# Performance work log

Measured on AMD Instinct MI355X. Metric: run time of the kernel, lower is better.

The kernel has to match this reference:

```python
import jax, jax.numpy as jnp
import numpy as np
import math

M, T, D, H, QK, K_ACT = 16, 512, 512, 512, 256, 4


def setup_inputs() -> dict:
    key = jax.random.key(0)
    ks = jax.random.split(key, 16)

    def xavier(k, shape):
        fan = shape[-1] + shape[-2]
        return jax.random.normal(k, shape, jnp.float32) * np.float32(math.sqrt(2.0 / fan))

    def bias(k, shape, fan_in):
        b = np.float32(1.0 / math.sqrt(fan_in))
        return jax.random.uniform(k, shape, jnp.float32, -b, b)

    return {
        "inputs": jax.random.normal(ks[0], (M, T, D), jnp.float32),
        # per-mechanism InputSelection params
        "Wq": xavier(ks[1], (M, QK, H)), "bq": bias(ks[2], (M, QK), H),
        "Wk": xavier(ks[3], (M, QK, D)), "bk": bias(ks[4], (M, QK), D),
        "Wv": xavier(ks[5], (M, D, D)), "bv": bias(ks[6], (M, D), D),
        # per-mechanism LSTMCell params (gate order i, f, g, o)
        "W_ih": xavier(ks[7], (M, 4 * H, D)), "b_ih": bias(ks[8], (M, 4 * H), H),
        "W_hh": xavier(ks[9], (M, 4 * H, H)), "b_hh": bias(ks[10], (M, 4 * H), H),
        # GroupLinearLayer weights for interaction attention
        "Wq_g": xavier(ks[11], (M, H, H)),
        "Wk_g": xavier(ks[12], (M, H, H)),
        "Wv_g": xavier(ks[13], (M, H, H)),
    }


def reference(inputs, Wq, bq, Wk, bk, Wv, bv, W_ih, b_ih, W_hh, b_hh, Wq_g, Wk_g, Wv_g):
    scale = 1.0 / math.sqrt(Wk.shape[1])  # 1/sqrt(key_size)
    xs = jnp.swapaxes(inputs, 0, 1)  # (T, M, D) for scan over time
    h0 = jnp.zeros((M, H), inputs.dtype)
    c0 = jnp.zeros((M, H), inputs.dtype)

    def step(carry, x_t):
        h, c = carry  # (M,H), (M,H)
        # --- InputSelection: augmented input rows are [zeros, x_t] ---
        q = jnp.einsum('mh,mqh->mq', h, Wq) + bq            # (M,QK)
        key_x = jnp.einsum('md,mkd->mk', x_t, Wk) + bk      # key of real input row
        logit0 = jnp.sum(q * bk, -1) * scale                # key of zero row == bias
        logit1 = jnp.sum(q * key_x, -1) * scale
        att = jax.nn.softmax(jnp.stack([logit0, logit1], -1), axis=-1)  # (M,2)
        val1 = jnp.einsum('md,mvd->mv', x_t, Wv) + bv       # (M,D)
        sel = att[:, 0:1] * bv + att[:, 1:2] * val1         # value of zero row == bias
        # --- top-k routing: smallest attention to the null input ---
        _, active_idx = jax.lax.top_k(-att[:, 0], K_ACT)
        mask = jnp.zeros((M,), inputs.dtype).at[active_idx].set(1.0)
        m = mask[:, None]
        # --- LSTMCell for all mechanisms, masked afterwards ---
        gates = (jnp.einsum('md,mgd->mg', sel, W_ih) + b_ih
                 + jnp.einsum('mh,mgh->mg', h, W_hh) + b_hh)  # (M,4H)
        i, f, g, o = jnp.split(gates, 4, axis=-1)
        c_new = jax.nn.sigmoid(f) * c + jax.nn.sigmoid(i) * jnp.tanh(g)
        h_new = jax.nn.sigmoid(o) * jnp.tanh(c_new)
        temp_h = m * h_new + (1 - m) * h
        new_c = m * c_new  # inactive cells are reset to zero (as in original)
        # --- interaction attention across mechanisms ---
        q2 = jnp.einsum('mh,mho->mo', temp_h, Wq_g)
        k2 = jnp.einsum('mh,mho->mo', temp_h, Wk_g)
        v2 = jnp.einsum('mh,mho->mo', temp_h, Wv_g)
        att2 = jax.nn.softmax(q2 @ k2.T, axis=1)            # (M,M), no sqrt scaling
        inter = (m * att2) @ v2                             # zero rows for inactive
        new_h = inter + (1 - m) * h + m * temp_h
        return (new_h, new_c), (new_h.reshape(-1), active_idx)

    _, (all_h, all_idx) = jax.lax.scan(step, (h0, c0), xs)
    return all_h, all_idx  # (T, M*H), (T, K_ACT)
```

## Files before the change

kernel.cpp:

```cpp
#include <hip/hip_runtime.h>

constexpr int M_ = 16, T_ = 512, D_ = 512, H_ = 512, QK_ = 256, G4_ = 2048;
constexpr float SCALE_ = 1.0f / 16.0f;

constexpr size_t KEY_OFF = 0;
constexpr size_t VAL_OFF = 2097152;
constexpr size_t H_OFF   = 6291456;
constexpr size_t C_OFF   = H_OFF + 8192;
constexpr size_t TH_OFF  = C_OFF + 8192;
constexpr size_t K2_OFF  = TH_OFF + 8192;
constexpr size_t V2_OFF  = K2_OFF + 8192;
constexpr size_t Q2_OFF  = V2_OFF + 8192;
constexpr size_t L0_OFF  = Q2_OFF + 2048;
constexpr size_t L1_OFF  = L0_OFF + 256;
constexpr size_t BAR_OFF = L1_OFF + 256;
constexpr int    BAR_WORDS = 16 * 32 + 32;

__device__ inline void load8f(const float* p, float f[8]) {
  float4 a = reinterpret_cast<const float4*>(p)[0];
  float4 b = reinterpret_cast<const float4*>(p)[1];
  f[0] = a.x; f[1] = a.y; f[2] = a.z; f[3] = a.w;
  f[4] = b.x; f[5] = b.y; f[6] = b.z; f[7] = b.w;
}

__device__ __forceinline__ float ldf(const float* p) {
  return __hip_atomic_load(p, __ATOMIC_RELAXED, __HIP_MEMORY_SCOPE_AGENT);
}
__device__ __forceinline__ void stf(float* p, float v) {
  __hip_atomic_store(p, v, __ATOMIC_RELAXED, __HIP_MEMORY_SCOPE_AGENT);
}
__device__ __forceinline__ float2 ldf2(const float* p) {
  unsigned long long u = __hip_atomic_load(
      reinterpret_cast<const unsigned long long*>(p),
      __ATOMIC_RELAXED, __HIP_MEMORY_SCOPE_AGENT);
  return __builtin_bit_cast(float2, u);
}
__device__ __forceinline__ void ld8f_cg(const float* p, float f[8]) {
  float2 a = ldf2(p), b = ldf2(p + 2), c = ldf2(p + 4), d = ldf2(p + 6);
  f[0] = a.x; f[1] = a.y; f[2] = b.x; f[3] = b.y;
  f[4] = c.x; f[5] = c.y; f[6] = d.x; f[7] = d.y;
}

__device__ inline float waveReduce(float v) {
#pragma unroll
  for (int d = 32; d > 0; d >>= 1) v += __shfl_xor(v, d);
  return v;
}

__device__ inline float sigm(float x) { return 1.f / (1.f + expf(-x)); }

__device__ __forceinline__ void gbar(float* wsf, unsigned idx) {
  unsigned* bar = reinterpret_cast<unsigned*>(wsf + BAR_OFF);
  asm volatile("s_waitcnt vmcnt(0)" ::: "memory");
  __syncthreads();
  if (threadIdx.x == 0) {
    const int sub = blockIdx.x >> 4;
    unsigned a = __hip_atomic_fetch_add(&bar[sub * 32], 1u, __ATOMIC_RELAXED,
                                        __HIP_MEMORY_SCOPE_AGENT);
    if (a == idx * 16u - 1u)
      __hip_atomic_fetch_add(&bar[512], 1u, __ATOMIC_RELAXED,
                             __HIP_MEMORY_SCOPE_AGENT);
    while (__hip_atomic_load(&bar[512], __ATOMIC_RELAXED,
                             __HIP_MEMORY_SCOPE_AGENT) < idx * 16u)
      __builtin_amdgcn_s_sleep(1);
  }
  __syncthreads();
  __builtin_amdgcn_sched_barrier(0);
}

__global__ void __launch_bounds__(256) keyval_kernel(
    const float* __restrict__ x, const float* __restrict__ Wk,
    const float* __restrict__ Wv, const float* __restrict__ bk,
    const float* __restrict__ bv, float* __restrict__ wsf) {
  __shared__ float Xs[64][33];
  __shared__ float Ws[64][33];
  int bid = blockIdx.x, tid = threadIdx.x;
  if (bid == 0) {
    for (int i = tid; i < BAR_WORDS; i += 256)
      reinterpret_cast<unsigned*>(wsf + BAR_OFF)[i] = 0u;
  }
  int m = bid / 96, r = bid % 96;
  int tt = r / 12, ot = r % 12;
  const float* xb = x + ((size_t)m * T_ + tt * 64) * D_;
  const float* wb; const float* bias; float* dst; int ld;
  if (ot < 4) {
    wb = Wk + (size_t)m * QK_ * D_ + (size_t)(ot * 64) * D_;
    bias = bk + m * QK_ + ot * 64;
    dst = wsf + KEY_OFF + ((size_t)m * T_ + tt * 64) * QK_ + ot * 64;
    ld = QK_;
  } else {
    wb = Wv + (size_t)m * D_ * D_ + (size_t)((ot - 4) * 64) * D_;
    bias = bv + m * D_ + (ot - 4) * 64;
    dst = wsf + VAL_OFF + ((size_t)m * T_ + tt * 64) * D_ + (ot - 4) * 64;
    ld = D_;
  }
  int lr = tid >> 2, lc = (tid & 3) * 8;
  int tx = tid & 15, ty = tid >> 4;
  float acc[4][4] = {};
  for (int k0 = 0; k0 < D_; k0 += 32) {
    float tmp[8];
    load8f(xb + (size_t)lr * D_ + k0 + lc, tmp);
#pragma unroll
    for (int i = 0; i < 8; ++i) Xs[lr][lc + i] = tmp[i];
    load8f(wb + (size_t)lr * D_ + k0 + lc, tmp);
#pragma unroll
    for (int i = 0; i < 8; ++i) Ws[lr][lc + i] = tmp[i];
    __syncthreads();
#pragma unroll
    for (int kk = 0; kk < 32; ++kk) {
      float xa[4], wv4[4];
#pragma unroll
      for (int a = 0; a < 4; ++a) xa[a] = Xs[ty * 4 + a][kk];
#pragma unroll
      for (int b = 0; b < 4; ++b) wv4[b] = Ws[tx * 4 + b][kk];
#pragma unroll
      for (int a = 0; a < 4; ++a)
#pragma unroll
        for (int b = 0; b < 4; ++b) acc[a][b] += xa[a] * wv4[b];
    }
    __syncthreads();
  }
#pragma unroll
  for (int b = 0; b < 4; ++b) {
    float bias_v = bias[tx * 4 + b];
#pragma unroll
    for (int a = 0; a < 4; ++a)
      dst[(size_t)(ty * 4 + a) * ld + tx * 4 + b] = acc[a][b] + bias_v;
  }
}

__global__ void __launch_bounds__(1024, 4) rim_main(
    const float* __restrict__ Wq, const float* __restrict__ bq,
    const float* __restrict__ bk, const float* __restrict__ bv,
    const float* __restrict__ Wih, const float* __restrict__ bih,
    const float* __restrict__ Whh, const float* __restrict__ bhh,
    const float* __restrict__ Wqg, const float* __restrict__ Wkg,
    const float* __restrict__ Wvg,
    float* __restrict__ wsf, float* __restrict__ out0, float* __restrict__ out1) {
  const int wg = blockIdx.x, tid = threadIdx.x;
  const int lane = tid & 63, wv = tid >> 6;
  const int m = wg >> 4, g = wg & 15;
  const int h32 = tid >> 5, oi = tid & 31;

  float* keyA = wsf + KEY_OFF;
  float* valA = wsf + VAL_OFF;
  float* hB  = wsf + H_OFF;
  float* cB  = wsf + C_OFF;
  float* thB = wsf + TH_OFF;
  float* k2B = wsf + K2_OFF;
  float* v2B = wsf + V2_OFF;
  float* q2B = wsf + Q2_OFF;
  float* l0B = wsf + L0_OFF;
  float* l1B = wsf + L1_OFF;

  __shared__ float s_newh[4][512];
  __shared__ float s_dv[512];
  __shared__ float s_pdk[16][32];
  __shared__ float s_pdv[16][32];
  __shared__ float s_pdq[16][32];
  __shared__ float s_l0[256];
  __shared__ float s_l1[256];
  __shared__ float s_small[64];
  __shared__ float s_w2[64];
  __shared__ float s_redA[16];
  __shared__ float s_redB[16];
  __shared__ float s_gv[4][8];

  float wqr[8], wkr[16], wvr[16];
  load8f(Wq + ((size_t)m * QK_ + g * 16 + wv) * H_ + lane * 8, wqr);
  {
    const size_t wo = ((size_t)m * H_ + h32 * 16) * H_ + g * 32 + oi;
#pragma unroll
    for (int i = 0; i < 16; ++i) wkr[i] = Wkg[wo + (size_t)i * H_];
#pragma unroll
    for (int i = 0; i < 16; ++i) wvr[i] = Wvg[wo + (size_t)i * H_];
  }
  const float qb = bq[m * QK_ + g * 16 + wv];
  const float kb = bk[m * QK_ + g * 16 + wv];

  unsigned bno = 0;

  if (g == 0 && tid < 512) {
    stf(hB + m * 512 + tid, 0.f);
    stf(cB + m * 512 + tid, 0.f);
  }
  gbar(wsf, ++bno);

  int p0 = 0, p1 = 0, p2 = 0, p3 = 0;
  int r0 = 0, r1 = 0, r2 = 0, r3 = 0;

  for (int t = 0; t <= T_; ++t) {
    int slot = -1;
    if (t > 0) {
      slot = (m == p0) ? 0 : (m == p1) ? 1 : (m == p2) ? 2 : (m == p3) ? 3 : -1;
      if (slot >= 0) {
        if (tid < 512) {
          int pr = tid >> 3, part = tid & 7;
          int s_ = pr >> 4, j_ = pr & 15;
          const float* q4 = q2B + s_ * 512 + part * 64;
          const float* k4 = k2B + j_ * 512 + part * 64;
          float acc = 0.f;
#pragma unroll
          for (int i = 0; i < 16; ++i) {
            float2 a0 = ldf2(q4 + i * 4), a1 = ldf2(q4 + i * 4 + 2);
            float2 b0 = ldf2(k4 + i * 4), b1 = ldf2(k4 + i * 4 + 2);
            acc += a0.x * b0.x + a0.y * b0.y + a1.x * b1.x + a1.y * b1.y;
          }
          acc += __shfl_xor(acc, 1);
          acc += __shfl_xor(acc, 2);
          acc += __shfl_xor(acc, 4);
          if (part == 0) s_small[pr] = acc;
        }
        __syncthreads();
        if (tid < 4) {
          float mx = -1e30f;
          for (int j = 0; j < 16; ++j) mx = fmaxf(mx, s_small[tid * 16 + j]);
          float sm = 0.f;
          for (int j = 0; j < 16; ++j) {
            float e = expf(s_small[tid * 16 + j] - mx);
            s_w2[tid * 16 + j] = e; sm += e;
          }
          float inv = 1.f / sm;
          for (int j = 0; j < 16; ++j) s_w2[tid * 16 + j] *= inv;
        }
        __syncthreads();
        {
          int s_ = tid >> 8, o0 = (tid & 255) * 2;
          float ax = 0.f, ay = 0.f;
#pragma unroll
          for (int j = 0; j < 16; ++j) {
            float w = s_w2[s_ * 16 + j];
            float2 v = ldf2(v2B + j * 512 + o0);
            ax += w * v.x; ay += w * v.y;
          }
          int myrow = s_ == 0 ? p0 : s_ == 1 ? p1 : s_ == 2 ? p2 : p3;
          float2 th = ldf2(thB + (size_t)myrow * 512 + o0);
          s_newh[s_][o0] = ax + th.x;
          s_newh[s_][o0 + 1] = ay + th.y;
        }
        __syncthreads();
      }
      if (g == 0 && tid < 512) {
        float v = (slot >= 0) ? s_newh[slot][tid] : ldf(hB + m * 512 + tid);
        out0[(size_t)(t - 1) * (M_ * H_) + m * 512 + tid] = v;
        if (slot >= 0) stf(hB + m * 512 + tid, v);
      }
    }
    if (t == T_) break;

    {
      float kv = keyA[((size_t)m * T_ + t) * QK_ + g * 16 + wv];
      float hreg[8];
      if (slot >= 0) {
#pragma unroll
        for (int i = 0; i < 8; ++i) hreg[i] = s_newh[slot][lane * 8 + i];
      } else {
        ld8f_cg(hB + m * 512 + lane * 8, hreg);
      }
      float acc = 0.f;
#pragma unroll
      for (int i = 0; i < 8; ++i) acc += hreg[i] * wqr[i];
      acc = waveReduce(acc);
      if (lane == 0) {
        float q = acc + qb;
        s_redA[wv] = q * kv;
        s_redB[wv] = q * kb;
      }
      __syncthreads();
      if (tid == 0) {
        float a = 0.f, b = 0.f;
        for (int w = 0; w < 16; ++w) { a += s_redA[w]; b += s_redB[w]; }
        stf(l1B + m * 16 + g, a);
        stf(l0B + m * 16 + g, b);
      }
    }
    gbar(wsf, ++bno);

    if (tid < 256) {
      s_l0[tid] = ldf(l0B + tid);
      s_l1[tid] = ldf(l1B + tid);
    }
    __syncthreads();
    if (tid < 16) {
      float l0 = 0.f, l1 = 0.f;
      for (int i = 0; i < 16; ++i) { l0 += s_l0[tid * 16 + i]; l1 += s_l1[tid * 16 + i]; }
      l0 *= SCALE_; l1 *= SCALE_;
      float mx = fmaxf(l0, l1);
      float e0 = expf(l0 - mx), e1 = expf(l1 - mx);
      float inv = 1.f / (e0 + e1);
      s_small[tid] = e0 * inv;
      s_small[16 + tid] = e1 * inv;
    }
    __syncthreads();
    {
      unsigned chosen = 0;
      int rr[4];
#pragma unroll
      for (int s = 0; s < 4; ++s) {
        float best = -2.f; int bm = 0;
        for (int mm = 0; mm < 16; ++mm) {
          if (chosen & (1u << mm)) continue;
          float v = -s_small[mm];
          if (v > best) { best = v; bm = mm; }
        }
        rr[s] = bm; chosen |= 1u << bm;
      }
      r0 = rr[0]; r1 = rr[1]; r2 = rr[2]; r3 = rr[3];
    }
    if (wg == 0 && tid < 4) {
      int rowv = tid == 0 ? r0 : tid == 1 ? r1 : tid == 2 ? r2 : r3;
      out1[(size_t)t * 4 + tid] = (float)rowv;
    }
    {
      int slot_c = wg >> 6, jc = wg & 63, j0 = jc * 8;
      int mA = slot_c == 0 ? r0 : slot_c == 1 ? r1 : slot_c == 2 ? r2 : r3;
      float a0v = s_small[mA], a1v = s_small[16 + mA];
      float bvr[8], vlr[8], hr[8];
      load8f(bv + mA * D_ + lane * 8, bvr);
      load8f(valA + ((size_t)mA * T_ + t) * D_ + lane * 8, vlr);
      ld8f_cg(hB + mA * 512 + lane * 8, hr);
      float selr[8];
#pragma unroll
      for (int i = 0; i < 8; ++i) selr[i] = a0v * bvr[i] + a1v * vlr[i];
#pragma unroll
      for (int u = 0; u < 2; ++u) {
        int gl = wv * 2 + u;
        int type = gl >> 3, jj = gl & 7;
        int gidx = type * 512 + j0 + jj;
        float wi[8], wh[8];
        load8f(Wih + ((size_t)mA * G4_ + gidx) * D_ + lane * 8, wi);
        load8f(Whh + ((size_t)mA * G4_ + gidx) * H_ + lane * 8, wh);
        float acc = 0.f;
#pragma unroll
        for (int k = 0; k < 8; ++k) acc += selr[k] * wi[k] + hr[k] * wh[k];
        acc = waveReduce(acc);
        if (lane == 0)
          s_gv[type][jj] = acc + bih[mA * G4_ + gidx] + bhh[mA * G4_ + gidx];
      }
      __syncthreads();
      if (tid < 8) {
        float gi = s_gv[0][tid], gf = s_gv[1][tid], gg = s_gv[2][tid], go = s_gv[3][tid];
        int j = j0 + tid;
        float cold = ldf(cB + mA * 512 + j);
        float cn = sigm(gf) * cold + sigm(gi) * tanhf(gg);
        float hn = sigm(go) * tanhf(cn);
        stf(cB + mA * 512 + j, cn);
        stf(thB + mA * 512 + j, hn);
      }
    }
    gbar(wsf, ++bno);

    {
      unsigned amask = (1u << r0) | (1u << r1) | (1u << r2) | (1u << r3);
      unsigned pmask = (1u << p0) | (1u << p1) | (1u << p2) | (1u << p3);
      bool act = (amask >> m) & 1;
      bool prevact = (t > 0) && ((pmask >> m) & 1);
      bool dirty = act || prevact || (t == 0);
      if (dirty) {
        const float* src = act ? thB + m * 512 : hB + m * 512;
        if (tid < 512) s_dv[tid] = ldf(src + tid);
        float wq2[16];
        int qslot = -1;
        if (act) {
          qslot = (m == r0) ? 0 : (m == r1) ? 1 : (m == r2) ? 2 : 3;
          const size_t wo = ((size_t)m * H_ + h32 * 16) * H_ + g * 32 + oi;
#pragma unroll
          for (int i = 0; i < 16; ++i) wq2[i] = Wqg[wo + (size_t)i * H_];
        }
        __syncthreads();
        float pk = 0.f, pv = 0.f, pq = 0.f;
#pragma unroll
        for (int i = 0; i < 16; ++i) {
          float s = s_dv[h32 * 16 + i];
          pk += s * wkr[i];
          pv += s * wvr[i];
        }
        if (act) {
#pragma unroll
          for (int i = 0; i < 16; ++i) pq += s_dv[h32 * 16 + i] * wq2[i];
        }
        pk += __shfl_xor(pk, 32);
        pv += __shfl_xor(pv, 32);
        pq += __shfl_xor(pq, 32);
        if (lane < 32) {
          s_pdk[wv][lane] = pk;
          s_pdv[wv][lane] = pv;
          s_pdq[wv][lane] = pq;
        }
        __syncthreads();
        if (tid < 32) {
          float a = 0.f, b = 0.f, c = 0.f;
          for (int w = 0; w < 16; ++w) {
            a += s_pdk[w][tid]; b += s_pdv[w][tid]; c += s_pdq[w][tid];
          }
          stf(k2B + m * 512 + g * 32 + tid, a);
          stf(v2B + m * 512 + g * 32 + tid, b);
          if (act) stf(q2B + qslot * 512 + g * 32 + tid, c);
        }
      }
      if (!act && prevact && g == 0 && tid < 512) stf(cB + m * 512 + tid, 0.f);
    }
    p0 = r0; p1 = r1; p2 = r2; p3 = r3;
    gbar(wsf, ++bno);
  }
}

extern "C" void kernel_launch(void* const* d_in, const int* in_sizes, int n_in,
                              void* d_out, int out_size, void* d_ws, size_t ws_size,
                              hipStream_t stream) {
  const float* x   = (const float*)d_in[0];
  const float* Wq  = (const float*)d_in[1];
  const float* bq  = (const float*)d_in[2];
  const float* Wk  = (const float*)d_in[3];
  const float* bk  = (const float*)d_in[4];
  const float* Wv  = (const float*)d_in[5];
  const float* bv  = (const float*)d_in[6];
  const float* Wih = (const float*)d_in[7];
  const float* bih = (const float*)d_in[8];
  const float* Whh = (const float*)d_in[9];
  const float* bhh = (const float*)d_in[10];
  const float* Wqg = (const float*)d_in[11];
  const float* Wkg = (const float*)d_in[12];
  const float* Wvg = (const float*)d_in[13];
  float* wsf = (float*)d_ws;
  float* out0 = (float*)d_out;
  float* out1 = out0 + (size_t)T_ * M_ * H_;
  (void)in_sizes; (void)n_in; (void)out_size; (void)ws_size;

  hipLaunchKernelGGL(keyval_kernel, dim3(1536), dim3(256), 0, stream,
                     x, Wk, Wv, bk, bv, wsf);

  void* kargs[] = {(void*)&Wq, (void*)&bq, (void*)&bk, (void*)&bv,
                   (void*)&Wih, (void*)&bih, (void*)&Whh, (void*)&bhh,
                   (void*)&Wqg, (void*)&Wkg, (void*)&Wvg,
                   (void*)&wsf, (void*)&out0, (void*)&out1};
  hipLaunchCooperativeKernel((void*)rim_main, dim3(256), dim3(1024), kargs, 0,
                             stream);
}
```

Measured before the change: 30.27 ms.

## Compute LSTM gates in each mechanism's own blocks with register-cached W_hh slice

Gate computation for the four active mechanisms is no longer spread across all 256 workgroups with dynamically chosen mechanisms. Each workgroup now computes only gates of its own mechanism m when that mechanism is active, handling 32 hidden units instead of 8. Half of the W_hh rows it needs are preloaded into registers once, before the time loop, which removes repeated global loads of W_hh. In exchange, work concentrates in the 64 workgroups of the active mechanisms (each doing 4x more rows), and the extra registers may lower occupancy.

```diff
diff --git a/kernel.cpp b/kernel.cpp
--- a/kernel.cpp
+++ b/kernel.cpp
@@ -164,7 +164,7 @@
   __shared__ float s_w2[64];
   __shared__ float s_redA[16];
   __shared__ float s_redB[16];
-  __shared__ float s_gv[4][8];
+  __shared__ float s_gv[4][32];
 
   float wqr[8], wkr[16], wvr[16];
   load8f(Wq + ((size_t)m * QK_ + g * 16 + wv) * H_ + lane * 8, wqr);
@@ -177,6 +177,13 @@
   }
   const float qb = bq[m * QK_ + g * 16 + wv];
   const float kb = bk[m * QK_ + g * 16 + wv];
+
+  const int typeC = wv >> 2;
+  const int gbaseC = typeC * 512 + g * 32 + (wv & 3) * 8;
+  float whr[4][8];
+#pragma unroll
+  for (int u = 0; u < 4; ++u)
+    load8f(Whh + ((size_t)m * G4_ + gbaseC + u) * H_ + lane * 8, whr[u]);
 
   unsigned bno = 0;
 
@@ -312,40 +319,54 @@
       out1[(size_t)t * 4 + tid] = (float)rowv;
     }
     {
-      int slot_c = wg >> 6, jc = wg & 63, j0 = jc * 8;
-      int mA = slot_c == 0 ? r0 : slot_c == 1 ? r1 : slot_c == 2 ? r2 : r3;
-      float a0v = s_small[mA], a1v = s_small[16 + mA];
-      float bvr[8], vlr[8], hr[8];
-      load8f(bv + mA * D_ + lane * 8, bvr);
-      load8f(valA + ((size_t)mA * T_ + t) * D_ + lane * 8, vlr);
-      ld8f_cg(hB + mA * 512 + lane * 8, hr);
-      float selr[8];
-#pragma unroll
-      for (int i = 0; i < 8; ++i) selr[i] = a0v * bvr[i] + a1v * vlr[i];
-#pragma unroll
-      for (int u = 0; u < 2; ++u) {
-        int gl = wv * 2 + u;
-        int type = gl >> 3, jj = gl & 7;
-        int gidx = type * 512 + j0 + jj;
-        float wi[8], wh[8];
-        load8f(Wih + ((size_t)mA * G4_ + gidx) * D_ + lane * 8, wi);
-        load8f(Whh + ((size_t)mA * G4_ + gidx) * H_ + lane * 8, wh);
-        float acc = 0.f;
-#pragma unroll
-        for (int k = 0; k < 8; ++k) acc += selr[k] * wi[k] + hr[k] * wh[k];
-        acc = waveReduce(acc);
-        if (lane == 0)
-          s_gv[type][jj] = acc + bih[mA * G4_ + gidx] + bhh[mA * G4_ + gidx];
-      }
-      __syncthreads();
-      if (tid < 8) {
-        float gi = s_gv[0][tid], gf = s_gv[1][tid], gg = s_gv[2][tid], go = s_gv[3][tid];
-        int j = j0 + tid;
-        float cold = ldf(cB + mA * 512 + j);
-        float cn = sigm(gf) * cold + sigm(gi) * tanhf(gg);
-        float hn = sigm(go) * tanhf(cn);
-        stf(cB + mA * 512 + j, cn);
-        stf(thB + mA * 512 + j, hn);
+      bool act = (m == r0) | (m == r1) | (m == r2) | (m == r3);
+      if (act) {
+        float a0v = s_small[m], a1v = s_small[16 + m];
+        float bvr[8], vlr[8], hr[8];
+        load8f(bv + m * D_ + lane * 8, bvr);
+        load8f(valA + ((size_t)m * T_ + t) * D_ + lane * 8, vlr);
+        ld8f_cg(hB + m * 512 + lane * 8, hr);
+        float selr[8];
+#pragma unroll
+        for (int i = 0; i < 8; ++i) selr[i] = a0v * bvr[i] + a1v * vlr[i];
+#pragma unroll
+        for (int u = 0; u < 4; ++u) {
+          int gidx = gbaseC + u;
+          float wi[8];
+          load8f(Wih + ((size_t)m * G4_ + gidx) * D_ + lane * 8, wi);
+          float acc = 0.f;
+#pragma unroll
+          for (int k = 0; k < 8; ++k) acc += selr[k] * wi[k] + hr[k] * whr[u][k];
+          acc = waveReduce(acc);
+          if (lane == 0)
+            s_gv[typeC][(wv & 3) * 8 + u] =
+                acc + bih[m * G4_ + gidx] + bhh[m * G4_ + gidx];
+        }
+#pragma unroll 2
+        for (int u = 4; u < 8; ++u) {
+          int gidx = gbaseC + u;
+          float wi[8], wh[8];
+          load8f(Wih + ((size_t)m * G4_ + gidx) * D_ + lane * 8, wi);
+          load8f(Whh + ((size_t)m * G4_ + gidx) * H_ + lane * 8, wh);
+          float acc = 0.f;
+#pragma unroll
+          for (int k = 0; k < 8; ++k) acc += selr[k] * wi[k] + hr[k] * wh[k];
+          acc = waveReduce(acc);
+          if (lane == 0)
+            s_gv[typeC][(wv & 3) * 8 + u] =
+                acc + bih[m * G4_ + gidx] + bhh[m * G4_ + gidx];
+        }
+        __syncthreads();
+        if (tid < 32) {
+          float gi = s_gv[0][tid], gf = s_gv[1][tid],
+                gg = s_gv[2][tid], go = s_gv[3][tid];
+          int j = g * 32 + tid;
+          float cold = ldf(cB + m * 512 + j);
+          float cn = sigm(gf) * cold + sigm(gi) * tanhf(gg);
+          float hn = sigm(go) * tanhf(cn);
+          stf(cB + m * 512 + j, cn);
+          stf(thB + m * 512 + j, hn);
+        }
       }
     }
     gbar(wsf, ++bno);
```

After: 41.17 ms. +36.0%, slower.
